# Optimization experiments

Measured on AMD Instinct MI355X. Metric: run time of the kernel, lower is better.

The kernel has to match this reference:

```python
import jax, jax.numpy as jnp
from jax import lax
import numpy as np

NUM_CLASSES = 80
STRIDE = 8
TOPK = 100
SIGAMA = 8.0


def setup_inputs() -> dict:
    key = jax.random.key(0)
    # raw head output: [B, 4+num_classes, H, W]
    x = jax.random.normal(key, (16, 4 + NUM_CLASSES, 160, 160), dtype=jnp.float32)
    return {"input": x}


def _decode(input):
    bs, attrs, H, W = input.shape
    C = attrs - 4
    pred = jnp.transpose(input, (0, 2, 3, 1))  # [B,H,W,4+C]
    x = jax.nn.sigmoid(pred[..., 0])
    y = jax.nn.sigmoid(pred[..., 1])
    w = pred[..., 2]
    h = pred[..., 3]
    pred_cls = jax.nn.sigmoid(pred[..., 4:])  # [B,H,W,C]

    grid_x = jnp.arange(W, dtype=input.dtype)[None, None, :]
    grid_y = jnp.arange(H, dtype=input.dtype)[None, :, None]
    pred_boxes = jnp.stack(
        [x + grid_x, y + grid_y, jnp.exp(w) * SIGAMA, jnp.exp(h) * SIGAMA], axis=-1
    )  # [B,H,W,4]

    # Faithful to F.max_pool2d applied to a [B,H,W,C] tensor: torch pools the
    # LAST TWO dims, i.e. a 5x5 window over (W, C), padding 2, stride 1.
    neg_inf = jnp.array(-jnp.inf, dtype=pred_cls.dtype)
    hmax = lax.reduce_window(
        pred_cls, neg_inf, lax.max,
        window_dimensions=(1, 1, 5, 5),
        window_strides=(1, 1, 1, 1),
        padding=((0, 0), (0, 0), (2, 2), (2, 2)),
    )
    keep = (hmax == pred_cls).astype(pred_cls.dtype)
    pred_cls = pred_cls * keep

    # --- dual top-k (CenterNet-style) ---
    scores = jnp.transpose(pred_cls, (0, 3, 1, 2)).reshape(bs, C, H * W)
    topk_scores, topk_inds = lax.top_k(scores, TOPK)          # [B,C,K] per-class
    topk_score, topk_ind = lax.top_k(topk_scores.reshape(bs, C * TOPK), TOPK)  # [B,K]
    topk_clses = (topk_ind // TOPK).astype(jnp.int32)         # class of each pick
    topk_inds = jnp.take_along_axis(topk_inds.reshape(bs, C * TOPK), topk_ind, axis=1)  # [B,K] spatial idx

    boxes = jnp.take_along_axis(
        pred_boxes.reshape(bs, H * W, 4), topk_inds[:, :, None], axis=1
    )  # [B,K,4]
    cls = jnp.take_along_axis(
        pred_cls.reshape(bs, H * W, C), topk_inds[:, :, None], axis=1
    )  # [B,K,C]
    conf = jnp.ones((bs, TOPK, 1), dtype=input.dtype)
    scale = jnp.array([STRIDE, STRIDE, STRIDE, STRIDE], dtype=input.dtype)
    return jnp.concatenate([boxes * scale, conf, cls], axis=-1)  # [B,K,5+C]


def reference(input):
    return _decode(input)
```

## Files before the change

### kernel.cpp

```cpp
#include <hip/hip_runtime.h>
#include <hip/hip_bf16.h>
#include <cstdint>

#define BATCH 16
#define ATTRS 84
#define NC    80
#define HH    160
#define WW    160
#define HWSZ  (HH * WW)
#define KTOP  100
#define CAP   8192
#define XGATE 2.9444389791664403f
#define LDW   92
#define LCAP  160
#define CSTR  16

__device__ __forceinline__ float sigf(float x) {
    return 1.0f / (1.0f + __expf(-x));
}

__global__ __launch_bounds__(320, 6) void k_nms(const float* __restrict__ in,
                                                unsigned long long* __restrict__ gather,
                                                unsigned int* __restrict__ counts) {
    const int wg = blockIdx.x;
    const int b  = wg / (HH * 2);
    const int hq = wg % (HH * 2);
    const int h  = hq >> 1;
    const int q  = hq & 1;
    const int t  = (int)threadIdx.x;

    __shared__ float sg[NC][LDW];
    __shared__ unsigned long long lbuf[LCAP];
    __shared__ unsigned int lcount;
    __shared__ unsigned int gbase;

    if (t == 0) lcount = 0;

    const int wb = q ? 76 : 0;
    const float* slab = in + ((size_t)b * ATTRS + 4) * HWSZ + (size_t)h * WW + wb;

    if (q == 0) {
#pragma unroll
        for (int it = 0; it < 6; ++it) {
            const int f4 = it * 320 + t;
            if (f4 < 1760) {
                const int c  = f4 / 22;
                const int j4 = f4 % 22;
                *reinterpret_cast<float4*>(&sg[c][j4 * 4]) =
                    *reinterpret_cast<const float4*>(slab + (size_t)c * HWSZ + j4 * 4);
            }
        }
    } else {
#pragma unroll
        for (int it = 0; it < 6; ++it) {
            const int f4 = it * 320 + t;
            if (f4 < 1680) {
                const int c  = f4 / 21;
                const int j4 = f4 % 21;
                *reinterpret_cast<float4*>(&sg[c][j4 * 4]) =
                    *reinterpret_cast<const float4*>(slab + (size_t)c * HWSZ + j4 * 4);
            }
        }
        if (t < NC) {
            float4 ni; ni.x = -INFINITY; ni.y = -INFINITY; ni.z = -INFINITY; ni.w = -INFINITY;
            *reinterpret_cast<float4*>(&sg[t][84]) = ni;
        }
    }
    __syncthreads();

    const int c   = t % NC;
    const int wq  = t / NC;
    const int cj0 = (q ? 4 : 0) + wq * 20;

    float4 v[7];
    if (cj0 >= 4) {
        v[0] = *reinterpret_cast<const float4*>(&sg[c][cj0 - 4]);
    } else {
        v[0].x = -INFINITY; v[0].y = -INFINITY; v[0].z = -INFINITY; v[0].w = -INFINITY;
    }
#pragma unroll
    for (int k = 1; k < 7; ++k) {
        v[k] = *reinterpret_cast<const float4*>(&sg[c][cj0 - 4 + 4 * k]);
    }
    float s_[28];
#pragma unroll
    for (int k = 0; k < 7; ++k) {
        s_[4 * k + 0] = v[k].x; s_[4 * k + 1] = v[k].y;
        s_[4 * k + 2] = v[k].z; s_[4 * k + 3] = v[k].w;
    }
    float hm[20];
#pragma unroll
    for (int i = 0; i < 20; ++i) {
        hm[i] = fmaxf(fmaxf(fmaxf(s_[i + 2], s_[i + 3]), fmaxf(s_[i + 4], s_[i + 5])), s_[i + 6]);
    }
    __syncthreads();

#pragma unroll
    for (int i = 0; i < 5; ++i) {
        float4 w4;
        w4.x = hm[4 * i + 0]; w4.y = hm[4 * i + 1];
        w4.z = hm[4 * i + 2]; w4.w = hm[4 * i + 3];
        *reinterpret_cast<float4*>(&sg[c][cj0 + 4 * i]) = w4;
    }
    __syncthreads();

    const int r0 = max(c - 2, 0), r1 = max(c - 1, 0);
    const int r3 = min(c + 1, NC - 1), r4 = min(c + 2, NC - 1);

#pragma unroll
    for (int qq = 0; qq < 5; ++qq) {
        const int j = cj0 + qq * 4;
        const float4 a0 = *reinterpret_cast<const float4*>(&sg[r0][j]);
        const float4 a1 = *reinterpret_cast<const float4*>(&sg[r1][j]);
        const float4 a2 = *reinterpret_cast<const float4*>(&sg[c ][j]);
        const float4 a3 = *reinterpret_cast<const float4*>(&sg[r3][j]);
        const float4 a4 = *reinterpret_cast<const float4*>(&sg[r4][j]);
#pragma unroll
        for (int jj = 0; jj < 4; ++jj) {
            const float v0 = (&a0.x)[jj], v1 = (&a1.x)[jj], v2 = (&a2.x)[jj];
            const float v3 = (&a3.x)[jj], v4 = (&a4.x)[jj];
            const float vm = fmaxf(fmaxf(fmaxf(v0, v1), fmaxf(v2, v3)), v4);
            const float sc = s_[4 + qq * 4 + jj];
            if (sc == vm && sc >= XGATE) {
                const float ssc = sigf(sc);
                const int w = wb + j + jj;
                const unsigned idx = (unsigned)(c * HWSZ + h * WW + w);
                unsigned long long key =
                    ((unsigned long long)__float_as_uint(ssc) << 21) |
                    (unsigned long long)(0x1FFFFFu - idx);
                unsigned p = atomicAdd(&lcount, 1u);
                if (p < LCAP) {
                    lbuf[p] = key;
                } else {
                    unsigned g = atomicAdd(&counts[b * CSTR], 1u);
                    if (g < CAP) gather[(size_t)b * CAP + g] = key;
                }
            }
        }
    }
    __syncthreads();

    const unsigned n = min(lcount, (unsigned)LCAP);
    if (t == 0 && n > 0) gbase = atomicAdd(&counts[b * CSTR], n);
    __syncthreads();
    for (unsigned i = t; i < n; i += 320) {
        unsigned g = gbase + i;
        if (g < CAP) gather[(size_t)b * CAP + g] = lbuf[i];
    }
}

__global__ __launch_bounds__(256) void k_select(const unsigned long long* __restrict__ gather,
                                                const unsigned int* __restrict__ counts,
                                                unsigned int* __restrict__ picks) {
    const int b = blockIdx.x;
    const int t = (int)threadIdx.x;

    __shared__ unsigned int hist[2048];
    __shared__ unsigned int chunksum[256];
    __shared__ unsigned long long compact[512];
    __shared__ unsigned int ncompact;
    __shared__ int b2_sh;

    const int M = min(counts[b * CSTR], (unsigned)CAP);
    const unsigned long long* keys = gather + (size_t)b * CAP;

    for (int i = t; i < 2048; i += 256) hist[i] = 0;
    if (t == 0) ncompact = 0;
    __syncthreads();

    for (int i = t; i < M; i += 256) {
        unsigned sb = (unsigned)(keys[i] >> 21);
        int bk = (int)((sb - 0x3F700000u) >> 9);
        bk = min(max(bk, 0), 2047);
        atomicAdd(&hist[bk], 1u);
    }
    __syncthreads();

    unsigned sum = 0;
#pragma unroll
    for (int j = 0; j < 8; ++j) sum += hist[t * 8 + j];
    chunksum[t] = sum;
    __syncthreads();
    for (int off = 1; off < 256; off <<= 1) {
        unsigned v = (t + off < 256) ? chunksum[t + off] : 0u;
        __syncthreads();
        chunksum[t] += v;
        __syncthreads();
    }

    const int target = (M < KTOP) ? M : KTOP;
    if (target > 0 &&
        (int)chunksum[t] >= target && (t == 255 || (int)chunksum[t + 1] < target)) {
        unsigned cum = (t == 255) ? 0u : chunksum[t + 1];
        int bsel = t * 8;
        for (int j = 7; j >= 0; --j) {
            cum += hist[t * 8 + j];
            if ((int)cum >= target) { bsel = t * 8 + j; break; }
        }
        b2_sh = bsel;
    }
    __syncthreads();
    const int b2 = b2_sh;

    for (int i = t; i < M; i += 256) {
        unsigned long long k = keys[i];
        unsigned sb = (unsigned)(k >> 21);
        int bk = min(max((int)((sb - 0x3F700000u) >> 9), 0), 2047);
        if (bk >= b2) {
            unsigned p = atomicAdd(&ncompact, 1u);
            if (p < 512) compact[p] = k;
        }
    }
    __syncthreads();

    const int N = (int)min(ncompact, 512u);
    for (int i = t; i < N; i += 256) {
        unsigned long long ki = compact[i];
        int rank = 0;
        for (int j = 0; j < N; ++j) rank += (compact[j] > ki) ? 1 : 0;
        if (rank < KTOP) {
            unsigned idx = 0x1FFFFFu - (unsigned)(ki & 0x1FFFFFu);
            picks[b * KTOP + rank] = idx % HWSZ;
        }
    }
}

__global__ __launch_bounds__(128) void k_emit(const float* __restrict__ in,
                                              const unsigned int* __restrict__ picks,
                                              float* __restrict__ out) {
    const int pk = blockIdx.x;
    const int b  = pk / KTOP;
    const int t  = (int)threadIdx.x;
    const unsigned hw = picks[pk];
    const int h = (int)(hw / WW), w = (int)(hw % WW);

    __shared__ float tile[NC][5];

    const float* base = in + (size_t)b * ATTRS * HWSZ;

    if (t < NC) {
        const int c = t;
        int a0 = (max(w - 2, 0)) & ~3;
        a0 = min(a0, WW - 8);
        const float* rp = base + (size_t)(4 + c) * HWSZ + (size_t)h * WW;
        const float4 f0 = *reinterpret_cast<const float4*>(rp + a0);
        const float4 f1 = *reinterpret_cast<const float4*>(rp + a0 + 4);
        float sp[8] = { f0.x, f0.y, f0.z, f0.w, f1.x, f1.y, f1.z, f1.w };
#pragma unroll
        for (int j = 0; j < 5; ++j) {
            const int wc = w + j - 2;
            float vv = -INFINITY;
            if (wc >= 0 && wc < WW) vv = sigf(sp[wc - a0]);
            tile[c][j] = vv;
        }
    }
    __syncthreads();

    float* orow = out + (size_t)pk * (5 + NC);

    if (t < 4) {
        float v = base[(size_t)t * HWSZ + hw];
        float r;
        if (t == 0)      r = (sigf(v) + (float)w) * 8.0f;
        else if (t == 1) r = (sigf(v) + (float)h) * 8.0f;
        else             r = expf(v) * 64.0f;
        orow[t] = r;
    }
    if (t == 4) orow[4] = 1.0f;

    if (t < NC) {
        const int c = t;
        const int cl = max(0, c - 2), ch = min(NC - 1, c + 2);
        float m = -INFINITY;
        for (int cc = cl; cc <= ch; ++cc) {
#pragma unroll
            for (int j = 0; j < 5; ++j) m = fmaxf(m, tile[cc][j]);
        }
        float sc = tile[c][2];
        orow[5 + c] = (sc == m) ? sc : 0.0f;
    }
}

extern "C" void kernel_launch(void* const* d_in, const int* in_sizes, int n_in,
                              void* d_out, int out_size, void* d_ws, size_t ws_size,
                              hipStream_t stream) {
    const float* in = (const float*)d_in[0];
    float* out = (float*)d_out;

    unsigned int* counts = (unsigned int*)d_ws;
    unsigned int* picks  = (unsigned int*)((char*)d_ws + 1024);
    unsigned long long* gather = (unsigned long long*)((char*)d_ws + 8192);

    hipMemsetAsync(d_ws, 0, 1024, stream);

    k_nms<<<BATCH * HH * 2, 320, 0, stream>>>(in, gather, counts);
    k_select<<<BATCH, 256, 0, stream>>>(gather, counts, picks);
    k_emit<<<BATCH * KTOP, 128, 0, stream>>>(in, picks, out);
}
```

Baseline: 218.3 us.

## Split NMS rows into quarters and compute 5x5 max only for gated candidates

The k_nms kernel now splits each row into four 40-wide column segments instead of two halves. This shrinks shared memory per block and allows higher occupancy (launch bounds raised to 8). The separable row-max pass, with its two extra barriers, is removed. The full 5x5 window max is now computed directly from shared memory, and only for elements that pass the sigmoid threshold gate. The trade-off is more blocks, a larger halo re-read fraction of input, and a per-candidate 25-element shared-memory scan.

```diff
diff --git a/kernel.cpp b/kernel.cpp
--- a/kernel.cpp
+++ b/kernel.cpp
@@ -11,23 +11,23 @@
 #define KTOP  100
 #define CAP   8192
 #define XGATE 2.9444389791664403f
-#define LDW   92
-#define LCAP  160
+#define LDW   48
+#define LCAP  64
 #define CSTR  16
 
 __device__ __forceinline__ float sigf(float x) {
     return 1.0f / (1.0f + __expf(-x));
 }
 
-__global__ __launch_bounds__(320, 6) void k_nms(const float* __restrict__ in,
+__global__ __launch_bounds__(320, 8) void k_nms(const float* __restrict__ in,
                                                 unsigned long long* __restrict__ gather,
                                                 unsigned int* __restrict__ counts) {
-    const int wg = blockIdx.x;
-    const int b  = wg / (HH * 2);
-    const int hq = wg % (HH * 2);
-    const int h  = hq >> 1;
-    const int q  = hq & 1;
-    const int t  = (int)threadIdx.x;
+    const int wg  = blockIdx.x;
+    const int b   = wg / (HH * 4);
+    const int rem = wg % (HH * 4);
+    const int h   = rem >> 2;
+    const int q   = rem & 3;
+    const int t   = (int)threadIdx.x;
 
     __shared__ float sg[NC][LDW];
     __shared__ unsigned long long lbuf[LCAP];
@@ -36,94 +36,58 @@
 
     if (t == 0) lcount = 0;
 
-    const int wb = q ? 76 : 0;
-    const float* slab = in + ((size_t)b * ATTRS + 4) * HWSZ + (size_t)h * WW + wb;
-
-    if (q == 0) {
-#pragma unroll
-        for (int it = 0; it < 6; ++it) {
-            const int f4 = it * 320 + t;
-            if (f4 < 1760) {
-                const int c  = f4 / 22;
-                const int j4 = f4 % 22;
-                *reinterpret_cast<float4*>(&sg[c][j4 * 4]) =
-                    *reinterpret_cast<const float4*>(slab + (size_t)c * HWSZ + j4 * 4);
-            }
-        }
-    } else {
-#pragma unroll
-        for (int it = 0; it < 6; ++it) {
-            const int f4 = it * 320 + t;
-            if (f4 < 1680) {
-                const int c  = f4 / 21;
-                const int j4 = f4 % 21;
-                *reinterpret_cast<float4*>(&sg[c][j4 * 4]) =
-                    *reinterpret_cast<const float4*>(slab + (size_t)c * HWSZ + j4 * 4);
-            }
-        }
-        if (t < NC) {
-            float4 ni; ni.x = -INFINITY; ni.y = -INFINITY; ni.z = -INFINITY; ni.w = -INFINITY;
-            *reinterpret_cast<float4*>(&sg[t][84]) = ni;
-        }
-    }
-    __syncthreads();
-
-    const int c   = t % NC;
-    const int wq  = t / NC;
-    const int cj0 = (q ? 4 : 0) + wq * 20;
-
-    float4 v[7];
-    if (cj0 >= 4) {
-        v[0] = *reinterpret_cast<const float4*>(&sg[c][cj0 - 4]);
-    } else {
-        v[0].x = -INFINITY; v[0].y = -INFINITY; v[0].z = -INFINITY; v[0].w = -INFINITY;
-    }
-#pragma unroll
-    for (int k = 1; k < 7; ++k) {
-        v[k] = *reinterpret_cast<const float4*>(&sg[c][cj0 - 4 + 4 * k]);
-    }
-    float s_[28];
+    const int w0 = q * 40;
+    const float* slab = in + ((size_t)b * ATTRS + 4) * HWSZ + (size_t)h * WW + (w0 - 4);
+
+#pragma unroll
+    for (int it = 0; it < 3; ++it) {
+        const int f4 = it * 320 + t;
+        const int c  = f4 / 12;
+        const int j4 = f4 % 12;
+        const bool oob = (q == 0 && j4 == 0) || (q == 3 && j4 == 11);
+        float4 v;
+        if (oob) {
+            v.x = -INFINITY; v.y = -INFINITY; v.z = -INFINITY; v.w = -INFINITY;
+        } else {
+            v = *reinterpret_cast<const float4*>(slab + (size_t)c * HWSZ + j4 * 4);
+        }
+        *reinterpret_cast<float4*>(&sg[c][j4 * 4]) = v;
+    }
+    __syncthreads();
+
+    const int c    = t % NC;
+    const int wq2  = t / NC;
+    const int cj0  = 4 + wq2 * 10;
+
+    float s_[14];
 #pragma unroll
     for (int k = 0; k < 7; ++k) {
-        s_[4 * k + 0] = v[k].x; s_[4 * k + 1] = v[k].y;
-        s_[4 * k + 2] = v[k].z; s_[4 * k + 3] = v[k].w;
-    }
-    float hm[20];
-#pragma unroll
-    for (int i = 0; i < 20; ++i) {
-        hm[i] = fmaxf(fmaxf(fmaxf(s_[i + 2], s_[i + 3]), fmaxf(s_[i + 4], s_[i + 5])), s_[i + 6]);
-    }
-    __syncthreads();
-
-#pragma unroll
-    for (int i = 0; i < 5; ++i) {
-        float4 w4;
-        w4.x = hm[4 * i + 0]; w4.y = hm[4 * i + 1];
-        w4.z = hm[4 * i + 2]; w4.w = hm[4 * i + 3];
-        *reinterpret_cast<float4*>(&sg[c][cj0 + 4 * i]) = w4;
-    }
-    __syncthreads();
+        const float2 v2 = *reinterpret_cast<const float2*>(&sg[c][cj0 - 2 + 2 * k]);
+        s_[2 * k + 0] = v2.x;
+        s_[2 * k + 1] = v2.y;
+    }
 
     const int r0 = max(c - 2, 0), r1 = max(c - 1, 0);
     const int r3 = min(c + 1, NC - 1), r4 = min(c + 2, NC - 1);
 
 #pragma unroll
-    for (int qq = 0; qq < 5; ++qq) {
-        const int j = cj0 + qq * 4;
-        const float4 a0 = *reinterpret_cast<const float4*>(&sg[r0][j]);
-        const float4 a1 = *reinterpret_cast<const float4*>(&sg[r1][j]);
-        const float4 a2 = *reinterpret_cast<const float4*>(&sg[c ][j]);
-        const float4 a3 = *reinterpret_cast<const float4*>(&sg[r3][j]);
-        const float4 a4 = *reinterpret_cast<const float4*>(&sg[r4][j]);
-#pragma unroll
-        for (int jj = 0; jj < 4; ++jj) {
-            const float v0 = (&a0.x)[jj], v1 = (&a1.x)[jj], v2 = (&a2.x)[jj];
-            const float v3 = (&a3.x)[jj], v4 = (&a4.x)[jj];
-            const float vm = fmaxf(fmaxf(fmaxf(v0, v1), fmaxf(v2, v3)), v4);
-            const float sc = s_[4 + qq * 4 + jj];
-            if (sc == vm && sc >= XGATE) {
-                const float ssc = sigf(sc);
-                const int w = wb + j + jj;
+    for (int i = 0; i < 10; ++i) {
+        const float x = s_[i + 2];
+        if (x >= XGATE) {
+            const int j = cj0 + i;
+            float vm = -INFINITY;
+#pragma unroll
+            for (int dj = -2; dj <= 2; ++dj) {
+                const int jj = j + dj;
+                vm = fmaxf(vm, sg[r0][jj]);
+                vm = fmaxf(vm, sg[r1][jj]);
+                vm = fmaxf(vm, sg[c ][jj]);
+                vm = fmaxf(vm, sg[r3][jj]);
+                vm = fmaxf(vm, sg[r4][jj]);
+            }
+            if (x == vm) {
+                const float ssc = sigf(x);
+                const int w = w0 + wq2 * 10 + i;
                 const unsigned idx = (unsigned)(c * HWSZ + h * WW + w);
                 unsigned long long key =
                     ((unsigned long long)__float_as_uint(ssc) << 21) |
@@ -293,7 +257,7 @@
 
     hipMemsetAsync(d_ws, 0, 1024, stream);
 
-    k_nms<<<BATCH * HH * 2, 320, 0, stream>>>(in, gather, counts);
+    k_nms<<<BATCH * HH * 4, 320, 0, stream>>>(in, gather, counts);
     k_select<<<BATCH, 256, 0, stream>>>(gather, counts, picks);
     k_emit<<<BATCH * KTOP, 128, 0, stream>>>(in, picks, out);
 }
```

Result: slower. 230.5 us (+5.6%).
